# Performance work log

Hardware: AMD Instinct MI355X
Metric: run time of the kernel (lower is better)

## Reference

```python
import jax, jax.numpy as jnp
import numpy as np

NUM_CLASSES = 10000
FEAT_DIM = 1024
BATCH = 4096


def setup_inputs() -> dict:
    key = jax.random.key(0)
    k1, k2 = jax.random.split(key)
    feat = jax.random.normal(k1, (BATCH, FEAT_DIM), dtype=jnp.float32)
    centers = jax.random.normal(k2, (NUM_CLASSES, FEAT_DIM), dtype=jnp.float32)
    return {"feat": feat, "centers": centers}


def reference(feat, centers):
    # logits = -0.5 * ||feat_b - center_c||^2, computed via the GEMM rewrite
    # ||a-b||^2 = ||a||^2 + ||b||^2 - 2 a.b  (same math as broadcast-sub-square-sum,
    # but avoids the [B, C, D] intermediate and uses tensor-core matmul).
    feat_sq = jnp.sum(feat * feat, axis=-1, keepdims=True)          # [B, 1]
    cent_sq = jnp.sum(centers * centers, axis=-1)[None, :]          # [1, C]
    cross = jnp.einsum('bd,cd->bc', feat, centers)                  # [B, C]
    dist = feat_sq + cent_sq - 2.0 * cross                          # [B, C]
    logits = -0.5 * dist
    return logits
```

## Files before the change

### kernel.cpp

```cpp
#include <hip/hip_runtime.h>
#include <hip/hip_bf16.h>
#include <stdint.h>

#define M_DIM 4096
#define N_DIM 10000
#define K_DIM 1024
#define GM (M_DIM / 128)
#define GN ((N_DIM + 127) / 128)
#define NT (K_DIM / 32)

typedef __attribute__((ext_vector_type(8))) short bf16x8;
typedef __attribute__((ext_vector_type(4))) float f32x4;

#define BAR()      asm volatile("s_barrier" ::: "memory")
#define WAITVM4()  asm volatile("s_waitcnt vmcnt(4)" ::: "memory")
#define WAITVM0()  asm volatile("s_waitcnt vmcnt(0)" ::: "memory")
#define WAITLGKM() asm volatile("s_waitcnt lgkmcnt(0)" ::: "memory")

__device__ __forceinline__ void async_ld16(const void* g, void* l) {
    __builtin_amdgcn_global_load_lds(
        (const __attribute__((address_space(1))) unsigned int*)g,
        (__attribute__((address_space(3))) unsigned int*)l,
        16, 0, 0);
}

__device__ __forceinline__ unsigned short f2bf(float f) {
    unsigned u = __float_as_uint(f);
    unsigned r = (u + 0x7FFFu + ((u >> 16) & 1u)) >> 16;
    return (unsigned short)r;
}

__global__ __launch_bounds__(256) void prep_rows(
    const float* __restrict__ feat, const float* __restrict__ cent,
    unsigned short* __restrict__ featbf, unsigned short* __restrict__ centbf,
    float* __restrict__ fsq, float* __restrict__ csq)
{
    const int wlane = threadIdx.x & 63;
    const int wid   = blockIdx.x * 4 + (threadIdx.x >> 6);
    const int nw    = gridDim.x * 4;
    for (int row = wid; row < M_DIM + N_DIM; row += nw) {
        const float* in;
        unsigned short* outb;
        float* sqp;
        if (row < M_DIM) {
            in = feat + (size_t)row * K_DIM;
            outb = featbf + (size_t)row * K_DIM;
            sqp = fsq + row;
        } else {
            const int r2 = row - M_DIM;
            in = cent + (size_t)r2 * K_DIM;
            outb = centbf + (size_t)r2 * K_DIM;
            sqp = csq + r2;
        }
        float s = 0.f;
        #pragma unroll
        for (int c = 0; c < 4; c++) {
            float4 v = ((const float4*)in)[wlane + c * 64];
            ushort4 pk;
            pk.x = f2bf(v.x); pk.y = f2bf(v.y); pk.z = f2bf(v.z); pk.w = f2bf(v.w);
            ((ushort4*)outb)[wlane + c * 64] = pk;
            s += v.x * v.x + v.y * v.y + v.z * v.z + v.w * v.w;
        }
        #pragma unroll
        for (int off = 32; off > 0; off >>= 1) s += __shfl_down(s, off, 64);
        if (wlane == 0) *sqp = s;
    }
}

__global__ __launch_bounds__(256, 4) void gemm_bt(
    const unsigned short* __restrict__ A,
    const unsigned short* __restrict__ B,
    const float* __restrict__ fsq, const float* __restrict__ csq,
    float* __restrict__ out)
{
    __shared__ unsigned short smem[16384];

    const int tid  = threadIdx.x;
    const int lane = tid & 63;
    const int wave = tid >> 6;
    const int wm = wave & 1;
    const int wn = wave >> 1;
    const int mlane = lane & 15;
    const int quad  = lane >> 4;
    const int qx  = (quad ^ ((mlane >> 1) & 3)) << 4;

    const int bid = blockIdx.x;
    const int xcd = bid & 7;
    const int idx = bid >> 3;
    const int r0  = xcd * 316 + idx;
    const int bm  = r0 & 31;
    const int bn  = r0 >> 5;

    const int arow_base = bm * 128;
    const int brow_base = bn * 128;

    const unsigned short* gA[2];
    const unsigned short* gB[2];
    int ldsA[2], ldsB[2];
    #pragma unroll
    for (int i = 0; i < 2; i++) {
        const int s   = i * 256 + tid;
        const int row = s >> 2;
        const int sc  = s & 3;
        const int kof = (sc ^ ((row >> 1) & 3)) << 3;
        gA[i] = A + (size_t)(arow_base + row) * K_DIM + kof;
        int br = brow_base + row; if (br > N_DIM - 1) br = N_DIM - 1;
        gB[i] = B + (size_t)br * K_DIM + kof;
        ldsA[i] = s * 16;
        ldsB[i] = 8192 + s * 16;
    }

    #define STAGE(t2, nbb)                                                    \
        do {                                                                  \
            async_ld16(gA[0] + (size_t)(t2) * 32, (char*)smem + (nbb) + ldsA[0]); \
            async_ld16(gA[1] + (size_t)(t2) * 32, (char*)smem + (nbb) + ldsA[1]); \
            async_ld16(gB[0] + (size_t)(t2) * 32, (char*)smem + (nbb) + ldsB[0]); \
            async_ld16(gB[1] + (size_t)(t2) * 32, (char*)smem + (nbb) + ldsB[1]); \
        } while (0)

    f32x4 acc[4][4];
    #pragma unroll
    for (int i = 0; i < 4; i++)
        #pragma unroll
        for (int j = 0; j < 4; j++) {
            f32x4 z = {0.f, 0.f, 0.f, 0.f};
            acc[i][j] = z;
        }

    const int aBase = (wm * 64 + mlane) * 64 + qx;
    const int bBase = 8192 + (wn * 64 + mlane) * 64 + qx;

    STAGE(0, 0);

    for (int t = 0; t < NT; ++t) {
        const char* base = (const char*)smem + (t & 1) * 16384;
        const int  nb    = ((t + 1) & 1) * 16384;
        if (t + 1 < NT) { STAGE(t + 1, nb); WAITVM4(); }
        else            { WAITVM0(); }
        BAR();

        bf16x8 af[4], bfv[4];
        #pragma unroll
        for (int i = 0; i < 4; i++) {
            af[i]  = *(const bf16x8*)(base + aBase + i * 1024);
            bfv[i] = *(const bf16x8*)(base + bBase + i * 1024);
        }
        __builtin_amdgcn_s_setprio(1);
        #pragma unroll
        for (int i = 0; i < 4; i++)
            #pragma unroll
            for (int j = 0; j < 4; j++)
                acc[i][j] = __builtin_amdgcn_mfma_f32_16x16x32_bf16(
                    af[i], bfv[j], acc[i][j], 0, 0, 0);
        __builtin_amdgcn_s_setprio(0);
        BAR();
    }
    #undef STAGE

    float* W = (float*)smem + wave * 1088;
    const int rbase0 = arow_base + wm * 64;
    const int cbase  = brow_base + wn * 64 + mlane;
    const int rb_col4 = mlane * 4;
    const int gcol4  = brow_base + wn * 64 + rb_col4;
    const bool colok = gcol4 < N_DIM;

    #pragma unroll
    for (int i = 0; i < 4; i++) {
        float frow[4];
        #pragma unroll
        for (int r = 0; r < 4; r++)
            frow[r] = -0.5f * fsq[rbase0 + i * 16 + quad * 4 + r];
        #pragma unroll
        for (int j = 0; j < 4; j++) {
            int col = cbase + j * 16;
            float cs = -0.5f * csq[col < N_DIM ? col : (N_DIM - 1)];
            #pragma unroll
            for (int r = 0; r < 4; r++)
                W[(quad * 4 + r) * 68 + j * 16 + mlane] = acc[i][j][r] + frow[r] + cs;
        }
        WAITLGKM();
        #pragma unroll
        for (int s = 0; s < 4; s++) {
            int rl = s * 4 + quad;
            f32x4 v = *(const f32x4*)&W[rl * 68 + rb_col4];
            if (colok) {
                int grow = rbase0 + i * 16 + rl;
                __builtin_nontemporal_store(v, (f32x4*)&out[(size_t)grow * N_DIM + gcol4]);
            }
        }
        WAITLGKM();
    }
}

extern "C" void kernel_launch(void* const* d_in, const int* in_sizes, int n_in,
                              void* d_out, int out_size, void* d_ws, size_t ws_size,
                              hipStream_t stream) {
    const float* feat = (const float*)d_in[0];
    const float* cent = (const float*)d_in[1];
    float* out = (float*)d_out;

    char* ws = (char*)d_ws;
    unsigned short* featbf = (unsigned short*)ws;
    unsigned short* centbf = (unsigned short*)(ws + 8388608);
    float* fsq = (float*)(ws + 8388608 + 20480000);
    float* csq = (float*)(ws + 8388608 + 20480000 + 16384);

    prep_rows<<<1024, 256, 0, stream>>>(feat, cent, featbf, centbf, fsq, csq);

    gemm_bt<<<GM * GN, 256, 0, stream>>>(featbf, centbf, fsq, csq, out);
}
```

Measured before the change: 303.6 us.

## Triple-buffer LDS K-tiles and remap GEMM tiles to per-XCD column bands

Result: faster. 290.3 us (-4.4%).

```diff
diff --git a/kernel.cpp b/kernel.cpp
--- a/kernel.cpp
+++ b/kernel.cpp
@@ -73,7 +73,7 @@
     const float* __restrict__ fsq, const float* __restrict__ csq,
     float* __restrict__ out)
 {
-    __shared__ unsigned short smem[16384];
+    __shared__ unsigned short smem[24576];
 
     const int tid  = threadIdx.x;
     const int lane = tid & 63;
@@ -86,10 +86,11 @@
 
     const int bid = blockIdx.x;
     const int xcd = bid & 7;
-    const int idx = bid >> 3;
-    const int r0  = xcd * 316 + idx;
-    const int bm  = r0 & 31;
-    const int bn  = r0 >> 5;
+    const int k   = bid >> 3;
+    const int W   = (xcd < 7) ? 10 : 9;
+    if (k >= 32 * W) return;
+    const int bm  = k / W;
+    const int bn  = ((xcd < 7) ? xcd * 10 : 70) + (k - bm * W);
 
     const int arow_base = bm * 128;
     const int brow_base = bn * 128;
@@ -131,14 +132,18 @@
     const int bBase = 8192 + (wn * 64 + mlane) * 64 + qx;
 
     STAGE(0, 0);
-
+    STAGE(1, 16384);
+    WAITVM4();
+    BAR();
+
+    int cur = 0;
+    int prv = 32768;
     for (int t = 0; t < NT; ++t) {
-        const char* base = (const char*)smem + (t & 1) * 16384;
-        const int  nb    = ((t + 1) & 1) * 16384;
-        if (t + 1 < NT) { STAGE(t + 1, nb); WAITVM4(); }
-        else            { WAITVM0(); }
+        if (t + 2 < NT) { STAGE(t + 2, prv); WAITVM4(); }
+        else if (t == NT - 2) { WAITVM0(); }
         BAR();
 
+        const char* base = (const char*)smem + cur;
         bf16x8 af[4], bfv[4];
         #pragma unroll
         for (int i = 0; i < 4; i++) {
@@ -154,10 +159,13 @@
                     af[i], bfv[j], acc[i][j], 0, 0, 0);
         __builtin_amdgcn_s_setprio(0);
         BAR();
+
+        int nxt = cur + 16384; if (nxt > 32768) nxt = 0;
+        prv = cur; cur = nxt;
     }
     #undef STAGE
 
-    float* W = (float*)smem + wave * 1088;
+    float* W2 = (float*)smem + wave * 1088;
     const int rbase0 = arow_base + wm * 64;
     const int cbase  = brow_base + wn * 64 + mlane;
     const int rb_col4 = mlane * 4;
@@ -176,13 +184,13 @@
             float cs = -0.5f * csq[col < N_DIM ? col : (N_DIM - 1)];
             #pragma unroll
             for (int r = 0; r < 4; r++)
-                W[(quad * 4 + r) * 68 + j * 16 + mlane] = acc[i][j][r] + frow[r] + cs;
+                W2[(quad * 4 + r) * 68 + j * 16 + mlane] = acc[i][j][r] + frow[r] + cs;
         }
         WAITLGKM();
         #pragma unroll
         for (int s = 0; s < 4; s++) {
             int rl = s * 4 + quad;
-            f32x4 v = *(const f32x4*)&W[rl * 68 + rb_col4];
+            f32x4 v = *(const f32x4*)&W2[rl * 68 + rb_col4];
             if (colok) {
                 int grow = rbase0 + i * 16 + rl;
                 __builtin_nontemporal_store(v, (f32x4*)&out[(size_t)grow * N_DIM + gcol4]);
@@ -207,5 +215,5 @@
 
     prep_rows<<<1024, 256, 0, stream>>>(feat, cent, featbf, centbf, fsq, csq);
 
-    gemm_bt<<<GM * GN, 256, 0, stream>>>(featbf, centbf, fsq, csq, out);
-}
+    gemm_bt<<<2560, 256, 0, stream>>>(featbf, centbf, fsq, csq, out);
+}
```
